# Kernel optimization log

Measured on AMD Instinct MI355X. Metric: run time of the kernel, lower is better.

## Reference

```python
import jax, jax.numpy as jnp
import numpy as np

B, NH, NKV, HD, SW, D = 32, 32, 8, 128, 4096, 4096
G = NH // NKV  # GQA group size


def setup_inputs() -> dict:
    key = jax.random.key(0)
    ks = jax.random.split(key, 7)
    x = jax.random.normal(ks[0], (1, 1, B, D), jnp.float32)
    wqkv = jax.random.normal(ks[1], (D, NH * HD + 2 * NKV * HD), jnp.float32) * 0.02
    wo = jax.random.normal(ks[2], (D, D), jnp.float32) * 0.02
    rot_mat = jax.random.normal(ks[3], (HD, HD), jnp.float32) * 0.1
    cache_k = jax.random.normal(ks[4], (B, NKV, SW, HD), jnp.float32)
    cache_v = jax.random.normal(ks[5], (B, NKV, SW, HD), jnp.float32)
    attn_mask = jnp.zeros((1, NH, B, SW), jnp.float32)
    return {"x": x, "wqkv": wqkv, "wo": wo, "rot_mat": rot_mat,
            "cache_k": cache_k, "cache_v": cache_v,
            "attn_mask": attn_mask, "current_pos": 4095}


def reference(x, wqkv, wo, rot_mat, cache_k, cache_v, attn_mask, current_pos):
    # start_pos advanced to 4096 -> padded_layer_past_len = layer_slice = SW (full window)
    scale = jnp.asarray(HD, x.dtype) ** -0.5
    # fused QKV projection: (B, D) @ (D, 6144)
    xqkv = x[0, 0] @ wqkv  # (B, NH*HD + 2*NKV*HD)
    q = xqkv[:, : NH * HD].reshape(B, NH, HD)
    k = xqkv[:, NH * HD: NH * HD + NKV * HD].reshape(B, NKV, HD)
    v = xqkv[:, NH * HD + NKV * HD:].reshape(B, NKV, HD)
    # matrix-form rotary embedding for the current position
    q = q @ rot_mat  # (B, NH, HD)
    k = k @ rot_mat  # (B, NKV, HD)
    # KV-cache update at current_pos
    keys = cache_k.at[:, :, current_pos, :].set(k)    # (B, NKV, SW, HD)
    values = cache_v.at[:, :, current_pos, :].set(v)  # (B, NKV, SW, HD)
    # GQA sliding-window attention over the (full) window
    qg = (q * scale).reshape(B, NKV, G, HD)
    scores = jnp.einsum('bkgd,bksd->bkgs', qg, keys)  # (B, NKV, G, SW)
    mask = jnp.transpose(attn_mask[0], (1, 0, 2)).reshape(B, NKV, G, SW)
    probs = jax.nn.softmax(scores + mask, axis=-1)
    ctx = jnp.einsum('bkgs,bksd->bkgd', probs, values)  # (B, NKV, G, HD)
    # concatenate heads + output projection
    out = ctx.reshape(B, NH * HD) @ wo  # (B, D)
    return out.reshape(1, 1, B, D)
```

## Files before the change

### kernel.cpp

```cpp
#include <hip/hip_runtime.h>

#define BB 32
#define NHH 32
#define NKVV 8
#define HDD 128
#define SWW 4096
#define DD 4096
#define GG 4
#define QKVC 6144
#define NSPLIT 16
#define CHUNK (SWW / NSPLIT)
#define KSPB 16

__global__ __launch_bounds__(256) void skinny_gemm_part(
    const float* __restrict__ x, const float* __restrict__ w,
    float* __restrict__ part, int K, int ncols) {
  __shared__ float2 red[4][64][8];
  const int t = threadIdx.x;
  const int ct = t & 63, kg = t >> 6;
  const long c0 = (long)blockIdx.x * 128 + ct * 2;
  const int Kb = K / KSPB;
  const int klen = Kb / 4;
  const int k0 = blockIdx.y * Kb + kg * klen;
  float2 acc[BB];
#pragma unroll
  for (int r = 0; r < BB; ++r) acc[r] = make_float2(0.f, 0.f);

#pragma unroll 2
  for (int k = k0; k < k0 + klen; k += 4) {
    float2 wv0 = *(const float2*)&w[(long)(k + 0) * ncols + c0];
    float2 wv1 = *(const float2*)&w[(long)(k + 1) * ncols + c0];
    float2 wv2 = *(const float2*)&w[(long)(k + 2) * ncols + c0];
    float2 wv3 = *(const float2*)&w[(long)(k + 3) * ncols + c0];
#pragma unroll
    for (int r = 0; r < BB; ++r) {
      float4 xv = *(const float4*)&x[r * K + k];
      acc[r].x = fmaf(xv.x, wv0.x, acc[r].x);
      acc[r].y = fmaf(xv.x, wv0.y, acc[r].y);
      acc[r].x = fmaf(xv.y, wv1.x, acc[r].x);
      acc[r].y = fmaf(xv.y, wv1.y, acc[r].y);
      acc[r].x = fmaf(xv.z, wv2.x, acc[r].x);
      acc[r].y = fmaf(xv.z, wv2.y, acc[r].y);
      acc[r].x = fmaf(xv.w, wv3.x, acc[r].x);
      acc[r].y = fmaf(xv.w, wv3.y, acc[r].y);
    }
  }
  for (int rc = 0; rc < 4; ++rc) {
    if (rc) __syncthreads();
#pragma unroll
    for (int j = 0; j < 8; ++j) red[kg][ct][j] = acc[rc * 8 + j];
    __syncthreads();
    if (kg == 0) {
#pragma unroll
      for (int j = 0; j < 8; ++j) {
        float2 s0 = red[0][ct][j], s1 = red[1][ct][j];
        float2 s2 = red[2][ct][j], s3 = red[3][ct][j];
        float2 sm = make_float2((s0.x + s1.x) + (s2.x + s3.x),
                                (s0.y + s1.y) + (s2.y + s3.y));
        *(float2*)&part[((long)blockIdx.y * BB + rc * 8 + j) * ncols + c0] = sm;
      }
    }
  }
}

__global__ __launch_bounds__(256) void reduce_part(
    const float* __restrict__ part, float* __restrict__ out, long n) {
  long i = (long)blockIdx.x * 256 + threadIdx.x;
  if (i >= n) return;
  float s = 0.f;
#pragma unroll
  for (int j = 0; j < KSPB; ++j) s += part[(long)j * n + i];
  out[i] = s;
}

__global__ __launch_bounds__(128) void rotary_kernel(
    const float* __restrict__ xqkv, const float* __restrict__ rot,
    float* __restrict__ q_rot, float* __restrict__ k_rot) {
  __shared__ float vec[HDD];
  const int blk = blockIdx.x;
  const int j = threadIdx.x;
  const float* src;
  float* dst;
  if (blk < BB * NHH) {
    int b = blk >> 5, h = blk & 31;
    src = xqkv + (long)b * QKVC + h * HDD;
    dst = q_rot + (long)(b * NHH + h) * HDD;
  } else {
    int i = blk - BB * NHH;
    int b = i >> 3, kv = i & 7;
    src = xqkv + (long)b * QKVC + NHH * HDD + kv * HDD;
    dst = k_rot + (long)(b * NKVV + kv) * HDD;
  }
  vec[j] = src[j];
  __syncthreads();
  float a0 = 0.f, a1 = 0.f, a2 = 0.f, a3 = 0.f;
#pragma unroll
  for (int d0 = 0; d0 < HDD; d0 += 4) {
    a0 += vec[d0 + 0] * rot[(d0 + 0) * HDD + j];
    a1 += vec[d0 + 1] * rot[(d0 + 1) * HDD + j];
    a2 += vec[d0 + 2] * rot[(d0 + 2) * HDD + j];
    a3 += vec[d0 + 3] * rot[(d0 + 3) * HDD + j];
  }
  dst[j] = (a0 + a1) + (a2 + a3);
}

__global__ __launch_bounds__(256) void attn_fused(
    const float* __restrict__ q_rot, const float* __restrict__ k_rot,
    const float* __restrict__ xqkv, const float* __restrict__ cache_k,
    const float* __restrict__ cache_v, const float* __restrict__ mask,
    const int* __restrict__ curpos, float* __restrict__ pm,
    float* __restrict__ pl, float* __restrict__ pacc) {
  __shared__ float4 mkp[CHUNK];
  __shared__ float wacc[4][GG][HDD];
  __shared__ float wml[4][GG][2];

  const int blk = blockIdx.x;
  const int split = blk & (NSPLIT - 1);
  const int bkv = blk >> 4;
  const int b = bkv >> 3, kv = bkv & 7;
  const int cur = curpos[0];
  const int s0 = split * CHUNK;
  const int t = threadIdx.x, lane = t & 63, w = t >> 6;
  const int lg = lane & 15;
  const int grp = lane >> 4;
  const float scale = 0.08838834764831845f;

  for (int i = t; i < GG * CHUNK; i += 256) {
    int g = i >> 8;
    int sl = i & (CHUNK - 1);
    ((float*)mkp)[sl * 4 + g] =
        mask[((long)(kv * GG + g) * BB + b) * SWW + s0 + sl];
  }

  float4 qa[GG], qb[GG];
#pragma unroll
  for (int g = 0; g < GG; ++g) {
    const float4* qp =
        (const float4*)(q_rot + (long)((b * NHH + kv * GG + g) * HDD));
    qa[g] = qp[lg];
    qb[g] = qp[lg + 16];
  }
  const float* kbase = cache_k + (long)(b * NKVV + kv) * SWW * HDD;
  const float* knew = k_rot + (long)(b * NKVV + kv) * HDD;
  const float* vbase = cache_v + (long)(b * NKVV + kv) * SWW * HDD;
  const float* vnew = xqkv + (long)b * QKVC + NHH * HDD + NKVV * HDD + kv * HDD;
  __syncthreads();

  float m0 = -1e30f, m1 = -1e30f, m2 = -1e30f, m3 = -1e30f;
  float l0 = 0.f, l1 = 0.f, l2 = 0.f, l3 = 0.f;
  float2 ac0 = make_float2(0, 0), ac1 = ac0, ac2 = ac0, ac3 = ac0;
  const int d = lane * 2;

  for (int it = 0; it < 16; ++it) {
    const int sloc = w * 64 + it * 4 + grp;
    const int s = s0 + sloc;
    const float4* kp =
        (const float4*)((s == cur) ? knew : (kbase + (long)s * HDD));
    float4 ka = kp[lg];
    float4 kb = kp[lg + 16];
    const int sb = s0 + w * 64 + it * 4;
    const float* vr0 = (sb + 0 == cur) ? vnew : (vbase + (long)(sb + 0) * HDD);
    const float* vr1 = (sb + 1 == cur) ? vnew : (vbase + (long)(sb + 1) * HDD);
    const float* vr2 = (sb + 2 == cur) ? vnew : (vbase + (long)(sb + 2) * HDD);
    const float* vr3 = (sb + 3 == cur) ? vnew : (vbase + (long)(sb + 3) * HDD);
    float2 v0 = *(const float2*)(vr0 + d);
    float2 v1 = *(const float2*)(vr1 + d);
    float2 v2 = *(const float2*)(vr2 + d);
    float2 v3 = *(const float2*)(vr3 + d);

    float dots[GG];
#pragma unroll
    for (int g = 0; g < GG; ++g) {
      dots[g] = ka.x * qa[g].x + ka.y * qa[g].y + ka.z * qa[g].z +
                ka.w * qa[g].w + kb.x * qb[g].x + kb.y * qb[g].y +
                kb.z * qb[g].z + kb.w * qb[g].w;
    }
#pragma unroll
    for (int mm = 1; mm < 16; mm <<= 1) {
#pragma unroll
      for (int g = 0; g < GG; ++g) dots[g] += __shfl_xor(dots[g], mm);
    }
    float4 mv = mkp[sloc];
    float4 sv;
    sv.x = fmaf(dots[0], scale, mv.x);
    sv.y = fmaf(dots[1], scale, mv.y);
    sv.z = fmaf(dots[2], scale, mv.z);
    sv.w = fmaf(dots[3], scale, mv.w);
    float4 sj0, sj1, sj2, sj3;
    sj0.x = __shfl(sv.x, 0);  sj0.y = __shfl(sv.y, 0);
    sj0.z = __shfl(sv.z, 0);  sj0.w = __shfl(sv.w, 0);
    sj1.x = __shfl(sv.x, 16); sj1.y = __shfl(sv.y, 16);
    sj1.z = __shfl(sv.z, 16); sj1.w = __shfl(sv.w, 16);
    sj2.x = __shfl(sv.x, 32); sj2.y = __shfl(sv.y, 32);
    sj2.z = __shfl(sv.z, 32); sj2.w = __shfl(sv.w, 32);
    sj3.x = __shfl(sv.x, 48); sj3.y = __shfl(sv.y, 48);
    sj3.z = __shfl(sv.z, 48); sj3.w = __shfl(sv.w, 48);
    float nm0 = fmaxf(fmaxf(sj0.x, sj1.x), fmaxf(sj2.x, sj3.x));
    float nm1 = fmaxf(fmaxf(sj0.y, sj1.y), fmaxf(sj2.y, sj3.y));
    float nm2 = fmaxf(fmaxf(sj0.z, sj1.z), fmaxf(sj2.z, sj3.z));
    float nm3 = fmaxf(fmaxf(sj0.w, sj1.w), fmaxf(sj2.w, sj3.w));
    if (nm0 > m0 + 8.f || nm1 > m1 + 8.f || nm2 > m2 + 8.f ||
        nm3 > m3 + 8.f) {
      float M2, f;
      M2 = fmaxf(m0, nm0); f = __expf(m0 - M2);
      l0 *= f; ac0.x *= f; ac0.y *= f; m0 = M2;
      M2 = fmaxf(m1, nm1); f = __expf(m1 - M2);
      l1 *= f; ac1.x *= f; ac1.y *= f; m1 = M2;
      M2 = fmaxf(m2, nm2); f = __expf(m2 - M2);
      l2 *= f; ac2.x *= f; ac2.y *= f; m2 = M2;
      M2 = fmaxf(m3, nm3); f = __expf(m3 - M2);
      l3 *= f; ac3.x *= f; ac3.y *= f; m3 = M2;
    }
    float p00 = __expf(sj0.x - m0), p10 = __expf(sj1.x - m0),
          p20 = __expf(sj2.x - m0), p30 = __expf(sj3.x - m0);
    float p01 = __expf(sj0.y - m1), p11 = __expf(sj1.y - m1),
          p21 = __expf(sj2.y - m1), p31 = __expf(sj3.y - m1);
    float p02 = __expf(sj0.z - m2), p12 = __expf(sj1.z - m2),
          p22 = __expf(sj2.z - m2), p32 = __expf(sj3.z - m2);
    float p03 = __expf(sj0.w - m3), p13 = __expf(sj1.w - m3),
          p23 = __expf(sj2.w - m3), p33 = __expf(sj3.w - m3);
    l0 += (p00 + p10) + (p20 + p30);
    l1 += (p01 + p11) + (p21 + p31);
    l2 += (p02 + p12) + (p22 + p32);
    l3 += (p03 + p13) + (p23 + p33);
    ac0.x = fmaf(p00, v0.x, fmaf(p10, v1.x, fmaf(p20, v2.x, fmaf(p30, v3.x, ac0.x))));
    ac0.y = fmaf(p00, v0.y, fmaf(p10, v1.y, fmaf(p20, v2.y, fmaf(p30, v3.y, ac0.y))));
    ac1.x = fmaf(p01, v0.x, fmaf(p11, v1.x, fmaf(p21, v2.x, fmaf(p31, v3.x, ac1.x))));
    ac1.y = fmaf(p01, v0.y, fmaf(p11, v1.y, fmaf(p21, v2.y, fmaf(p31, v3.y, ac1.y))));
    ac2.x = fmaf(p02, v0.x, fmaf(p12, v1.x, fmaf(p22, v2.x, fmaf(p32, v3.x, ac2.x))));
    ac2.y = fmaf(p02, v0.y, fmaf(p12, v1.y, fmaf(p22, v2.y, fmaf(p32, v3.y, ac2.y))));
    ac3.x = fmaf(p03, v0.x, fmaf(p13, v1.x, fmaf(p23, v2.x, fmaf(p33, v3.x, ac3.x))));
    ac3.y = fmaf(p03, v0.y, fmaf(p13, v1.y, fmaf(p23, v2.y, fmaf(p33, v3.y, ac3.y))));
  }

  wacc[w][0][d] = ac0.x; wacc[w][0][d + 1] = ac0.y;
  wacc[w][1][d] = ac1.x; wacc[w][1][d + 1] = ac1.y;
  wacc[w][2][d] = ac2.x; wacc[w][2][d + 1] = ac2.y;
  wacc[w][3][d] = ac3.x; wacc[w][3][d + 1] = ac3.y;
  if (lane == 0) {
    wml[w][0][0] = m0; wml[w][0][1] = l0;
    wml[w][1][0] = m1; wml[w][1][1] = l1;
    wml[w][2][0] = m2; wml[w][2][1] = l2;
    wml[w][3][0] = m3; wml[w][3][1] = l3;
  }
  __syncthreads();

  {
    const int g = t >> 6;
    const int dd = (t & 63) * 2;
    float Mg = fmaxf(fmaxf(wml[0][g][0], wml[1][g][0]),
                     fmaxf(wml[2][g][0], wml[3][g][0]));
    float Lg = 0.f, a0 = 0.f, a1 = 0.f;
#pragma unroll
    for (int ww = 0; ww < 4; ++ww) {
      float f = __expf(wml[ww][g][0] - Mg);
      Lg = fmaf(wml[ww][g][1], f, Lg);
      a0 = fmaf(f, wacc[ww][g][dd], a0);
      a1 = fmaf(f, wacc[ww][g][dd + 1], a1);
    }
    const long pidx = ((long)(b * NHH + kv * GG + g)) * NSPLIT + split;
    pacc[pidx * HDD + dd] = a0;
    pacc[pidx * HDD + dd + 1] = a1;
    if ((t & 63) == 0) {
      pm[pidx] = Mg;
      pl[pidx] = Lg;
    }
  }
}

__global__ __launch_bounds__(128) void attn_combine(
    const float* __restrict__ pm, const float* __restrict__ pl,
    const float* __restrict__ pacc, float* __restrict__ ctx) {
  const int bh = blockIdx.x;
  const int d = threadIdx.x;
  float M = -1e30f;
#pragma unroll
  for (int i = 0; i < NSPLIT; ++i) M = fmaxf(M, pm[bh * NSPLIT + i]);
  float L = 0.f, a = 0.f;
#pragma unroll
  for (int i = 0; i < NSPLIT; ++i) {
    float wexp = __expf(pm[bh * NSPLIT + i] - M);
    L += pl[bh * NSPLIT + i] * wexp;
    a += wexp * pacc[((long)bh * NSPLIT + i) * HDD + d];
  }
  ctx[(long)bh * HDD + d] = a / L;
}

extern "C" void kernel_launch(void* const* d_in, const int* in_sizes, int n_in,
                              void* d_out, int out_size, void* d_ws,
                              size_t ws_size, hipStream_t stream) {
  const float* x = (const float*)d_in[0];
  const float* wqkv = (const float*)d_in[1];
  const float* wo = (const float*)d_in[2];
  const float* rot = (const float*)d_in[3];
  const float* cache_k = (const float*)d_in[4];
  const float* cache_v = (const float*)d_in[5];
  const float* mask = (const float*)d_in[6];
  const int* curpos = (const int*)d_in[7];
  float* out = (float*)d_out;

  float* ws = (float*)d_ws;
  float* xqkv = ws;
  float* q_rot = xqkv + 196608;
  float* k_rot = q_rot + 131072;
  float* pm = k_rot + 32768;
  float* pl = pm + 16384;
  float* ctx = pl + 16384;
  float* big = ctx + 131072;
  (void)in_sizes; (void)n_in; (void)out_size; (void)ws_size;

  hipLaunchKernelGGL(skinny_gemm_part, dim3(QKVC / 128, KSPB), dim3(256), 0,
                     stream, x, wqkv, big, DD, QKVC);
  hipLaunchKernelGGL(reduce_part, dim3((BB * QKVC) / 256), dim3(256), 0,
                     stream, big, xqkv, (long)BB * QKVC);
  hipLaunchKernelGGL(rotary_kernel, dim3(BB * NHH + BB * NKVV), dim3(128), 0,
                     stream, xqkv, rot, q_rot, k_rot);
  hipLaunchKernelGGL(attn_fused, dim3(BB * NKVV * NSPLIT), dim3(256), 0,
                     stream, q_rot, k_rot, xqkv, cache_k, cache_v, mask,
                     curpos, pm, pl, big);
  hipLaunchKernelGGL(attn_combine, dim3(BB * NHH), dim3(128), 0, stream, pm,
                     pl, big, ctx);
  hipLaunchKernelGGL(skinny_gemm_part, dim3(DD / 128, KSPB), dim3(256), 0,
                     stream, ctx, wo, big, DD, DD);
  hipLaunchKernelGGL(reduce_part, dim3((BB * DD) / 256), dim3(256), 0, stream,
                     big, out, (long)BB * DD);
}
```

Before: 383.1 us.

## Split fused flash-decode attention into QK, exact softmax, and PV kernels

Replaces the single online-softmax attention kernel with three passes: a QK-scores kernel that writes raw scores to global memory, a per-row softmax kernel that applies scale and mask, and a PV kernel that streams V with float4 loads and sums plain partials. This drops the running-max rescaling, the per-step shuffle broadcasts and the heavy exp work from the bandwidth-bound KV loop, and the combine step becomes a simple sum. In exchange it adds two kernel launches and a round trip of the score matrix through global memory (about 16 MB written and read).

```diff
diff --git a/kernel.cpp b/kernel.cpp
--- a/kernel.cpp
+++ b/kernel.cpp
@@ -11,6 +11,7 @@
 #define NSPLIT 16
 #define CHUNK (SWW / NSPLIT)
 #define KSPB 16
+#define SCALE 0.08838834764831845f
 
 __global__ __launch_bounds__(256) void skinny_gemm_part(
     const float* __restrict__ x, const float* __restrict__ w,
@@ -104,16 +105,11 @@
   dst[j] = (a0 + a1) + (a2 + a3);
 }
 
-__global__ __launch_bounds__(256) void attn_fused(
+__global__ __launch_bounds__(256) void qk_scores(
     const float* __restrict__ q_rot, const float* __restrict__ k_rot,
-    const float* __restrict__ xqkv, const float* __restrict__ cache_k,
-    const float* __restrict__ cache_v, const float* __restrict__ mask,
-    const int* __restrict__ curpos, float* __restrict__ pm,
-    float* __restrict__ pl, float* __restrict__ pacc) {
-  __shared__ float4 mkp[CHUNK];
-  __shared__ float wacc[4][GG][HDD];
-  __shared__ float wml[4][GG][2];
-
+    const float* __restrict__ cache_k, const int* __restrict__ curpos,
+    float* __restrict__ scores) {
+  __shared__ float sc[GG][CHUNK];
   const int blk = blockIdx.x;
   const int split = blk & (NSPLIT - 1);
   const int bkv = blk >> 4;
@@ -121,16 +117,7 @@
   const int cur = curpos[0];
   const int s0 = split * CHUNK;
   const int t = threadIdx.x, lane = t & 63, w = t >> 6;
-  const int lg = lane & 15;
-  const int grp = lane >> 4;
-  const float scale = 0.08838834764831845f;
-
-  for (int i = t; i < GG * CHUNK; i += 256) {
-    int g = i >> 8;
-    int sl = i & (CHUNK - 1);
-    ((float*)mkp)[sl * 4 + g] =
-        mask[((long)(kv * GG + g) * BB + b) * SWW + s0 + sl];
-  }
+  const int lg = lane & 15, grp = lane >> 4;
 
   float4 qa[GG], qb[GG];
 #pragma unroll
@@ -142,15 +129,8 @@
   }
   const float* kbase = cache_k + (long)(b * NKVV + kv) * SWW * HDD;
   const float* knew = k_rot + (long)(b * NKVV + kv) * HDD;
-  const float* vbase = cache_v + (long)(b * NKVV + kv) * SWW * HDD;
-  const float* vnew = xqkv + (long)b * QKVC + NHH * HDD + NKVV * HDD + kv * HDD;
-  __syncthreads();
-
-  float m0 = -1e30f, m1 = -1e30f, m2 = -1e30f, m3 = -1e30f;
-  float l0 = 0.f, l1 = 0.f, l2 = 0.f, l3 = 0.f;
-  float2 ac0 = make_float2(0, 0), ac1 = ac0, ac2 = ac0, ac3 = ac0;
-  const int d = lane * 2;
-
+
+#pragma unroll 2
   for (int it = 0; it < 16; ++it) {
     const int sloc = w * 64 + it * 4 + grp;
     const int s = s0 + sloc;
@@ -158,16 +138,6 @@
         (const float4*)((s == cur) ? knew : (kbase + (long)s * HDD));
     float4 ka = kp[lg];
     float4 kb = kp[lg + 16];
-    const int sb = s0 + w * 64 + it * 4;
-    const float* vr0 = (sb + 0 == cur) ? vnew : (vbase + (long)(sb + 0) * HDD);
-    const float* vr1 = (sb + 1 == cur) ? vnew : (vbase + (long)(sb + 1) * HDD);
-    const float* vr2 = (sb + 2 == cur) ? vnew : (vbase + (long)(sb + 2) * HDD);
-    const float* vr3 = (sb + 3 == cur) ? vnew : (vbase + (long)(sb + 3) * HDD);
-    float2 v0 = *(const float2*)(vr0 + d);
-    float2 v1 = *(const float2*)(vr1 + d);
-    float2 v2 = *(const float2*)(vr2 + d);
-    float2 v3 = *(const float2*)(vr3 + d);
-
     float dots[GG];
 #pragma unroll
     for (int g = 0; g < GG; ++g) {
@@ -180,110 +150,157 @@
 #pragma unroll
       for (int g = 0; g < GG; ++g) dots[g] += __shfl_xor(dots[g], mm);
     }
-    float4 mv = mkp[sloc];
-    float4 sv;
-    sv.x = fmaf(dots[0], scale, mv.x);
-    sv.y = fmaf(dots[1], scale, mv.y);
-    sv.z = fmaf(dots[2], scale, mv.z);
-    sv.w = fmaf(dots[3], scale, mv.w);
-    float4 sj0, sj1, sj2, sj3;
-    sj0.x = __shfl(sv.x, 0);  sj0.y = __shfl(sv.y, 0);
-    sj0.z = __shfl(sv.z, 0);  sj0.w = __shfl(sv.w, 0);
-    sj1.x = __shfl(sv.x, 16); sj1.y = __shfl(sv.y, 16);
-    sj1.z = __shfl(sv.z, 16); sj1.w = __shfl(sv.w, 16);
-    sj2.x = __shfl(sv.x, 32); sj2.y = __shfl(sv.y, 32);
-    sj2.z = __shfl(sv.z, 32); sj2.w = __shfl(sv.w, 32);
-    sj3.x = __shfl(sv.x, 48); sj3.y = __shfl(sv.y, 48);
-    sj3.z = __shfl(sv.z, 48); sj3.w = __shfl(sv.w, 48);
-    float nm0 = fmaxf(fmaxf(sj0.x, sj1.x), fmaxf(sj2.x, sj3.x));
-    float nm1 = fmaxf(fmaxf(sj0.y, sj1.y), fmaxf(sj2.y, sj3.y));
-    float nm2 = fmaxf(fmaxf(sj0.z, sj1.z), fmaxf(sj2.z, sj3.z));
-    float nm3 = fmaxf(fmaxf(sj0.w, sj1.w), fmaxf(sj2.w, sj3.w));
-    if (nm0 > m0 + 8.f || nm1 > m1 + 8.f || nm2 > m2 + 8.f ||
-        nm3 > m3 + 8.f) {
-      float M2, f;
-      M2 = fmaxf(m0, nm0); f = __expf(m0 - M2);
-      l0 *= f; ac0.x *= f; ac0.y *= f; m0 = M2;
-      M2 = fmaxf(m1, nm1); f = __expf(m1 - M2);
-      l1 *= f; ac1.x *= f; ac1.y *= f; m1 = M2;
-      M2 = fmaxf(m2, nm2); f = __expf(m2 - M2);
-      l2 *= f; ac2.x *= f; ac2.y *= f; m2 = M2;
-      M2 = fmaxf(m3, nm3); f = __expf(m3 - M2);
-      l3 *= f; ac3.x *= f; ac3.y *= f; m3 = M2;
-    }
-    float p00 = __expf(sj0.x - m0), p10 = __expf(sj1.x - m0),
-          p20 = __expf(sj2.x - m0), p30 = __expf(sj3.x - m0);
-    float p01 = __expf(sj0.y - m1), p11 = __expf(sj1.y - m1),
-          p21 = __expf(sj2.y - m1), p31 = __expf(sj3.y - m1);
-    float p02 = __expf(sj0.z - m2), p12 = __expf(sj1.z - m2),
-          p22 = __expf(sj2.z - m2), p32 = __expf(sj3.z - m2);
-    float p03 = __expf(sj0.w - m3), p13 = __expf(sj1.w - m3),
-          p23 = __expf(sj2.w - m3), p33 = __expf(sj3.w - m3);
-    l0 += (p00 + p10) + (p20 + p30);
-    l1 += (p01 + p11) + (p21 + p31);
-    l2 += (p02 + p12) + (p22 + p32);
-    l3 += (p03 + p13) + (p23 + p33);
-    ac0.x = fmaf(p00, v0.x, fmaf(p10, v1.x, fmaf(p20, v2.x, fmaf(p30, v3.x, ac0.x))));
-    ac0.y = fmaf(p00, v0.y, fmaf(p10, v1.y, fmaf(p20, v2.y, fmaf(p30, v3.y, ac0.y))));
-    ac1.x = fmaf(p01, v0.x, fmaf(p11, v1.x, fmaf(p21, v2.x, fmaf(p31, v3.x, ac1.x))));
-    ac1.y = fmaf(p01, v0.y, fmaf(p11, v1.y, fmaf(p21, v2.y, fmaf(p31, v3.y, ac1.y))));
-    ac2.x = fmaf(p02, v0.x, fmaf(p12, v1.x, fmaf(p22, v2.x, fmaf(p32, v3.x, ac2.x))));
-    ac2.y = fmaf(p02, v0.y, fmaf(p12, v1.y, fmaf(p22, v2.y, fmaf(p32, v3.y, ac2.y))));
-    ac3.x = fmaf(p03, v0.x, fmaf(p13, v1.x, fmaf(p23, v2.x, fmaf(p33, v3.x, ac3.x))));
-    ac3.y = fmaf(p03, v0.y, fmaf(p13, v1.y, fmaf(p23, v2.y, fmaf(p33, v3.y, ac3.y))));
-  }
-
-  wacc[w][0][d] = ac0.x; wacc[w][0][d + 1] = ac0.y;
-  wacc[w][1][d] = ac1.x; wacc[w][1][d + 1] = ac1.y;
-  wacc[w][2][d] = ac2.x; wacc[w][2][d + 1] = ac2.y;
-  wacc[w][3][d] = ac3.x; wacc[w][3][d + 1] = ac3.y;
-  if (lane == 0) {
-    wml[w][0][0] = m0; wml[w][0][1] = l0;
-    wml[w][1][0] = m1; wml[w][1][1] = l1;
-    wml[w][2][0] = m2; wml[w][2][1] = l2;
-    wml[w][3][0] = m3; wml[w][3][1] = l3;
-  }
-  __syncthreads();
-
-  {
-    const int g = t >> 6;
-    const int dd = (t & 63) * 2;
-    float Mg = fmaxf(fmaxf(wml[0][g][0], wml[1][g][0]),
-                     fmaxf(wml[2][g][0], wml[3][g][0]));
-    float Lg = 0.f, a0 = 0.f, a1 = 0.f;
-#pragma unroll
-    for (int ww = 0; ww < 4; ++ww) {
-      float f = __expf(wml[ww][g][0] - Mg);
-      Lg = fmaf(wml[ww][g][1], f, Lg);
-      a0 = fmaf(f, wacc[ww][g][dd], a0);
-      a1 = fmaf(f, wacc[ww][g][dd + 1], a1);
-    }
-    const long pidx = ((long)(b * NHH + kv * GG + g)) * NSPLIT + split;
-    pacc[pidx * HDD + dd] = a0;
-    pacc[pidx * HDD + dd + 1] = a1;
-    if ((t & 63) == 0) {
-      pm[pidx] = Mg;
-      pl[pidx] = Lg;
-    }
-  }
-}
-
-__global__ __launch_bounds__(128) void attn_combine(
-    const float* __restrict__ pm, const float* __restrict__ pl,
+    if (lg == 0) {
+#pragma unroll
+      for (int g = 0; g < GG; ++g) sc[g][sloc] = dots[g];
+    }
+  }
+  __syncthreads();
+  for (int i = t; i < GG * CHUNK; i += 256) {
+    int g = i >> 8, sl = i & (CHUNK - 1);
+    scores[((long)(b * NHH + kv * GG + g)) * SWW + s0 + sl] = sc[g][sl];
+  }
+}
+
+__global__ __launch_bounds__(256) void softmax_row(
+    float* __restrict__ scores, const float* __restrict__ mask) {
+  __shared__ float red[4];
+  const int bh = blockIdx.x;
+  const int b = bh >> 5, h = bh & 31;
+  const int t = threadIdx.x, lane = t & 63, w = t >> 6;
+  float4* srow = (float4*)(scores + (long)bh * SWW);
+  const float4* mrow = (const float4*)(mask + ((long)h * BB + b) * SWW);
+  float4 e[4];
+  float mx = -1e30f;
+#pragma unroll
+  for (int j = 0; j < 4; ++j) {
+    float4 s4 = srow[t + j * 256];
+    float4 m4 = mrow[t + j * 256];
+    e[j].x = fmaf(s4.x, SCALE, m4.x);
+    e[j].y = fmaf(s4.y, SCALE, m4.y);
+    e[j].z = fmaf(s4.z, SCALE, m4.z);
+    e[j].w = fmaf(s4.w, SCALE, m4.w);
+    mx = fmaxf(mx, fmaxf(fmaxf(e[j].x, e[j].y), fmaxf(e[j].z, e[j].w)));
+  }
+#pragma unroll
+  for (int mm = 1; mm < 64; mm <<= 1) mx = fmaxf(mx, __shfl_xor(mx, mm));
+  if (lane == 0) red[w] = mx;
+  __syncthreads();
+  const float M = fmaxf(fmaxf(red[0], red[1]), fmaxf(red[2], red[3]));
+  float sum = 0.f;
+#pragma unroll
+  for (int j = 0; j < 4; ++j) {
+    e[j].x = __expf(e[j].x - M);
+    e[j].y = __expf(e[j].y - M);
+    e[j].z = __expf(e[j].z - M);
+    e[j].w = __expf(e[j].w - M);
+    sum += (e[j].x + e[j].y) + (e[j].z + e[j].w);
+  }
+#pragma unroll
+  for (int mm = 1; mm < 64; mm <<= 1) sum += __shfl_xor(sum, mm);
+  __syncthreads();
+  if (lane == 0) red[w] = sum;
+  __syncthreads();
+  const float L = (red[0] + red[1]) + (red[2] + red[3]);
+  const float rinv = 1.0f / L;
+#pragma unroll
+  for (int j = 0; j < 4; ++j) {
+    e[j].x *= rinv;
+    e[j].y *= rinv;
+    e[j].z *= rinv;
+    e[j].w *= rinv;
+    srow[t + j * 256] = e[j];
+  }
+}
+
+__global__ __launch_bounds__(256) void pv_partial(
+    const float* __restrict__ probs, const float* __restrict__ xqkv,
+    const float* __restrict__ cache_v, const int* __restrict__ curpos,
+    float* __restrict__ pacc) {
+  __shared__ float pr[GG][CHUNK];
+  __shared__ float wacc[4][GG][HDD];
+  const int blk = blockIdx.x;
+  const int split = blk & (NSPLIT - 1);
+  const int bkv = blk >> 4;
+  const int b = bkv >> 3, kv = bkv & 7;
+  const int cur = curpos[0];
+  const int s0 = split * CHUNK;
+  const int t = threadIdx.x, lane = t & 63, w = t >> 6;
+  const int par = lane >> 5, dl = lane & 31;
+
+  for (int i = t; i < GG * CHUNK; i += 256) {
+    int g = i >> 8, sl = i & (CHUNK - 1);
+    pr[g][sl] = probs[((long)(b * NHH + kv * GG + g)) * SWW + s0 + sl];
+  }
+  const float* vbase = cache_v + (long)(b * NKVV + kv) * SWW * HDD;
+  const float* vnew =
+      xqkv + (long)b * QKVC + NHH * HDD + NKVV * HDD + kv * HDD;
+  __syncthreads();
+
+  float4 a0 = make_float4(0, 0, 0, 0), a1 = a0, a2 = a0, a3 = a0;
+#pragma unroll 4
+  for (int it = 0; it < 32; ++it) {
+    const int slp = w * 64 + it * 2 + par;
+    const int s = s0 + slp;
+    const float4* vp =
+        (const float4*)((s == cur) ? vnew : (vbase + (long)s * HDD));
+    float4 v4 = vp[dl];
+    float p0 = pr[0][slp], p1 = pr[1][slp], p2 = pr[2][slp], p3 = pr[3][slp];
+    a0.x = fmaf(p0, v4.x, a0.x);
+    a0.y = fmaf(p0, v4.y, a0.y);
+    a0.z = fmaf(p0, v4.z, a0.z);
+    a0.w = fmaf(p0, v4.w, a0.w);
+    a1.x = fmaf(p1, v4.x, a1.x);
+    a1.y = fmaf(p1, v4.y, a1.y);
+    a1.z = fmaf(p1, v4.z, a1.z);
+    a1.w = fmaf(p1, v4.w, a1.w);
+    a2.x = fmaf(p2, v4.x, a2.x);
+    a2.y = fmaf(p2, v4.y, a2.y);
+    a2.z = fmaf(p2, v4.z, a2.z);
+    a2.w = fmaf(p2, v4.w, a2.w);
+    a3.x = fmaf(p3, v4.x, a3.x);
+    a3.y = fmaf(p3, v4.y, a3.y);
+    a3.z = fmaf(p3, v4.z, a3.z);
+    a3.w = fmaf(p3, v4.w, a3.w);
+  }
+  a0.x += __shfl_xor(a0.x, 32);
+  a0.y += __shfl_xor(a0.y, 32);
+  a0.z += __shfl_xor(a0.z, 32);
+  a0.w += __shfl_xor(a0.w, 32);
+  a1.x += __shfl_xor(a1.x, 32);
+  a1.y += __shfl_xor(a1.y, 32);
+  a1.z += __shfl_xor(a1.z, 32);
+  a1.w += __shfl_xor(a1.w, 32);
+  a2.x += __shfl_xor(a2.x, 32);
+  a2.y += __shfl_xor(a2.y, 32);
+  a2.z += __shfl_xor(a2.z, 32);
+  a2.w += __shfl_xor(a2.w, 32);
+  a3.x += __shfl_xor(a3.x, 32);
+  a3.y += __shfl_xor(a3.y, 32);
+  a3.z += __shfl_xor(a3.z, 32);
+  a3.w += __shfl_xor(a3.w, 32);
+  if (par == 0) {
+    *(float4*)&wacc[w][0][dl * 4] = a0;
+    *(float4*)&wacc[w][1][dl * 4] = a1;
+    *(float4*)&wacc[w][2][dl * 4] = a2;
+    *(float4*)&wacc[w][3][dl * 4] = a3;
+  }
+  __syncthreads();
+  for (int i = t; i < GG * HDD; i += 256) {
+    int g = i >> 7, dd = i & (HDD - 1);
+    float sv = (wacc[0][g][dd] + wacc[1][g][dd]) + (wacc[2][g][dd] + wacc[3][g][dd]);
+    pacc[(((long)(b * NHH + kv * GG + g)) * NSPLIT + split) * HDD + dd] = sv;
+  }
+}
+
+__global__ __launch_bounds__(128) void sum_combine(
     const float* __restrict__ pacc, float* __restrict__ ctx) {
   const int bh = blockIdx.x;
   const int d = threadIdx.x;
-  float M = -1e30f;
-#pragma unroll
-  for (int i = 0; i < NSPLIT; ++i) M = fmaxf(M, pm[bh * NSPLIT + i]);
-  float L = 0.f, a = 0.f;
-#pragma unroll
-  for (int i = 0; i < NSPLIT; ++i) {
-    float wexp = __expf(pm[bh * NSPLIT + i] - M);
-    L += pl[bh * NSPLIT + i] * wexp;
-    a += wexp * pacc[((long)bh * NSPLIT + i) * HDD + d];
-  }
-  ctx[(long)bh * HDD + d] = a / L;
+  float a = 0.f;
+#pragma unroll
+  for (int i = 0; i < NSPLIT; ++i) a += pacc[((long)bh * NSPLIT + i) * HDD + d];
+  ctx[(long)bh * HDD + d] = a;
 }
 
 extern "C" void kernel_launch(void* const* d_in, const int* in_sizes, int n_in,
@@ -303,10 +320,9 @@
   float* xqkv = ws;
   float* q_rot = xqkv + 196608;
   float* k_rot = q_rot + 131072;
-  float* pm = k_rot + 32768;
-  float* pl = pm + 16384;
-  float* ctx = pl + 16384;
-  float* big = ctx + 131072;
+  float* ctx = k_rot + 32768;
+  float* pacc = ctx + 131072;
+  float* big = pacc + 2097152;
   (void)in_sizes; (void)n_in; (void)out_size; (void)ws_size;
 
   hipLaunchKernelGGL(skinny_gemm_part, dim3(QKVC / 128, KSPB), dim3(256), 0,
@@ -315,11 +331,14 @@
                      stream, big, xqkv, (long)BB * QKVC);
   hipLaunchKernelGGL(rotary_kernel, dim3(BB * NHH + BB * NKVV), dim3(128), 0,
                      stream, xqkv, rot, q_rot, k_rot);
-  hipLaunchKernelGGL(attn_fused, dim3(BB * NKVV * NSPLIT), dim3(256), 0,
-                     stream, q_rot, k_rot, xqkv, cache_k, cache_v, mask,
-                     curpos, pm, pl, big);
-  hipLaunchKernelGGL(attn_combine, dim3(BB * NHH), dim3(128), 0, stream, pm,
-                     pl, big, ctx);
+  hipLaunchKernelGGL(qk_scores, dim3(BB * NKVV * NSPLIT), dim3(256), 0, stream,
+                     q_rot, k_rot, cache_k, curpos, big);
+  hipLaunchKernelGGL(softmax_row, dim3(BB * NHH), dim3(256), 0, stream, big,
+                     mask);
+  hipLaunchKernelGGL(pv_partial, dim3(BB * NKVV * NSPLIT), dim3(256), 0,
+                     stream, big, xqkv, cache_v, curpos, pacc);
+  hipLaunchKernelGGL(sum_combine, dim3(BB * NHH), dim3(128), 0, stream, pacc,
+                     ctx);
   hipLaunchKernelGGL(skinny_gemm_part, dim3(DD / 128, KSPB), dim3(256), 0,
                      stream, ctx, wo, big, DD, DD);
   hipLaunchKernelGGL(reduce_part, dim3((BB * DD) / 256), dim3(256), 0, stream,
```

Result: slower. 397.4 us (+3.7%).
